# Kernel optimization log

Measured on AMD Instinct MI355X. Metric: run time of the kernel, lower is better.

Reference implementation:

```python
import jax, jax.numpy as jnp
import numpy as np

# Model dims
E, K, D, F = 8, 2, 1024, 2048   # num_experts, top_k, d_model, d_ff
B, S = 2, 1024                  # batch, seq -> T = 2048 tokens


def setup_inputs() -> dict:
    key = jax.random.key(0)
    k1, k2, k3, k4 = jax.random.split(key, 4)
    hidden = jax.random.normal(k1, (B, S, D), dtype=jnp.float32)
    gate_logits = jax.random.normal(k2, (B * S, E), dtype=jnp.float32)
    # Expert FFN params: expert_e(x) = silu(x @ W1[e]) @ W2[e]
    W1 = jax.random.normal(k3, (E, D, F), dtype=jnp.float32) * 0.02
    W2 = jax.random.normal(k4, (E, F, D), dtype=jnp.float32) * 0.02
    return {"hidden": hidden, "gate_logits": gate_logits, "W1": W1, "W2": W2}


def reference(hidden, gate_logits, W1, W2):
    b, s, d = hidden.shape
    x = hidden.reshape(-1, d)                                  # [T, D]
    # Router: softmax -> top-k -> renormalize (gate_logits path of forward)
    probs = jax.nn.softmax(gate_logits, axis=-1)               # [T, E]
    topk_w, topk_idx = jax.lax.top_k(probs, K)                 # [T, K]
    topk_w = topk_w / jnp.sum(topk_w, axis=-1, keepdims=True)
    # Combine weights as a dense [T, E] map (top_k indices are distinct)
    tok_w = jnp.sum(jax.nn.one_hot(topk_idx, E, dtype=topk_w.dtype)
                    * topk_w[..., None], axis=1)               # [T, E]
    # Grouped expert FFN, expressed densely over the expert axis; the
    # combine weights zero out non-selected experts, so the math equals the
    # original gather -> per-expert GEMM -> weighted scatter-combine.
    h = jax.nn.silu(jnp.einsum('td,edf->tef', x, W1))          # [T, E, F]
    y = jnp.einsum('tef,efd->ted', h, W2)                      # [T, E, D]
    out = jnp.einsum('te,ted->td', tok_w, y)                   # [T, D]
    return out.reshape(b, s, d)
```

## Files before the change

kernel.cpp:

```cpp
#include <hip/hip_runtime.h>
#include <hip/hip_bf16.h>

#define E_N 8
#define D_DIM 1024
#define F_DIM 2048
#define T_N 2048
#define BM 128
#define BN 128
#define BK 32
#define LDP 40

typedef unsigned short u16;
typedef unsigned int u32;
typedef float floatx4 __attribute__((ext_vector_type(4)));
typedef short bf16x8v __attribute__((ext_vector_type(8)));

__device__ __forceinline__ u16 f2bf(float f) {
    union { float f; u32 u; } v; v.f = f;
    u32 r = v.u + 0x7FFFu + ((v.u >> 16) & 1u);
    return (u16)(r >> 16);
}

__global__ void router_kernel(const float* __restrict__ gl,
                              int* __restrict__ cnt, int* __restrict__ base,
                              int* __restrict__ slot_tok, int* __restrict__ tok_slot,
                              float* __restrict__ tok_w) {
    __shared__ int scnt[E_N];
    __shared__ int sbase[E_N];
    const int tid = threadIdx.x;
    if (tid < E_N) scnt[tid] = 0;
    __syncthreads();
    int e0a[8], e1a[8], p0a[8], p1a[8];
    float w0a[8];
#pragma unroll
    for (int i = 0; i < 8; ++i) {
        const int t = tid + i * 256;
        const float4* gp = (const float4*)(gl + (size_t)t * E_N);
        const float4 x0 = gp[0], x1 = gp[1];
        float l[E_N] = {x0.x, x0.y, x0.z, x0.w, x1.x, x1.y, x1.z, x1.w};
        int e0 = 0; float m0 = l[0];
#pragma unroll
        for (int e = 1; e < E_N; ++e) if (l[e] > m0) { m0 = l[e]; e0 = e; }
        int e1 = -1; float m1 = -1e30f;
#pragma unroll
        for (int e = 0; e < E_N; ++e) if (e != e0 && l[e] > m1) { m1 = l[e]; e1 = e; }
        const float p = __expf(m1 - m0);
        w0a[i] = 1.0f / (1.0f + p);
        e0a[i] = e0; e1a[i] = e1;
        p0a[i] = atomicAdd(&scnt[e0], 1);
        p1a[i] = atomicAdd(&scnt[e1], 1);
    }
    __syncthreads();
    if (tid == 0) {
        int s = 0;
        for (int e = 0; e < E_N; ++e) { sbase[e] = s; base[e] = s; cnt[e] = scnt[e]; s += scnt[e]; }
    }
    __syncthreads();
#pragma unroll
    for (int i = 0; i < 8; ++i) {
        const int t = tid + i * 256;
        const int s0 = sbase[e0a[i]] + p0a[i];
        const int s1 = sbase[e1a[i]] + p1a[i];
        slot_tok[s0] = t; slot_tok[s1] = t;
        tok_slot[2 * t] = s0; tok_slot[2 * t + 1] = s1;
        tok_w[2 * t] = w0a[i]; tok_w[2 * t + 1] = 1.0f - w0a[i];
    }
}

__global__ __launch_bounds__(256)
void gemm1_kernel(const float* __restrict__ X, const float* __restrict__ W1,
                  const int* __restrict__ cnt, const int* __restrict__ base,
                  const int* __restrict__ slot_tok, u16* __restrict__ h) {
    const int e = blockIdx.z, mt = blockIdx.y, ft = blockIdx.x;
    const int cnt_e = cnt[e];
    if (mt * BM >= cnt_e) return;
    const int base_e = base[e];
    __shared__ __align__(16) u16 Alds[BM][LDP];
    __shared__ __align__(16) u16 Blds[BN][LDP];
    const int tid = threadIdx.x;
    const int ar = tid >> 1, ah = tid & 1;
    const int arow_g = mt * BM + ar;
    const int tok = (arow_g < cnt_e) ? slot_tok[base_e + arow_g] : 0;
    const float* aptr = X + (size_t)tok * D_DIM + ah * 16;
    const int bfc = tid & 127, bh = tid >> 7;
    const float* bptr = W1 + (size_t)e * D_DIM * F_DIM + (size_t)(bh * 16) * F_DIM
                        + (size_t)ft * BN + bfc;
    const int wid = tid >> 6, lane = tid & 63;
    const int wm = (wid >> 1) * 64, wn = (wid & 1) * 64;
    const int lr = lane & 15, lk = (lane >> 4) * 8;
    floatx4 acc[4][4];
    const floatx4 zero = {0.f, 0.f, 0.f, 0.f};
#pragma unroll
    for (int i = 0; i < 4; ++i)
#pragma unroll
        for (int j = 0; j < 4; ++j) acc[i][j] = zero;

    for (int kt = 0; kt < D_DIM / BK; ++kt) {
        const int k0 = kt * BK;
        float4 av[4];
#pragma unroll
        for (int c = 0; c < 4; ++c) av[c] = *(const float4*)(aptr + k0 + c * 4);
        float bv[16];
#pragma unroll
        for (int kk = 0; kk < 16; ++kk) bv[kk] = bptr[(size_t)(k0 + kk) * F_DIM];
        __syncthreads();
        u32 ua[8], ub[8];
#pragma unroll
        for (int c = 0; c < 4; ++c) {
            ua[2 * c]     = (u32)f2bf(av[c].x) | ((u32)f2bf(av[c].y) << 16);
            ua[2 * c + 1] = (u32)f2bf(av[c].z) | ((u32)f2bf(av[c].w) << 16);
        }
#pragma unroll
        for (int j = 0; j < 8; ++j)
            ub[j] = (u32)f2bf(bv[2 * j]) | ((u32)f2bf(bv[2 * j + 1]) << 16);
        u32* adst = (u32*)&Alds[ar][ah * 16];
        *(uint4*)(adst)     = make_uint4(ua[0], ua[1], ua[2], ua[3]);
        *(uint4*)(adst + 4) = make_uint4(ua[4], ua[5], ua[6], ua[7]);
        u32* bdst = (u32*)&Blds[bfc][bh * 16];
        *(uint4*)(bdst)     = make_uint4(ub[0], ub[1], ub[2], ub[3]);
        *(uint4*)(bdst + 4) = make_uint4(ub[4], ub[5], ub[6], ub[7]);
        __syncthreads();
        bf16x8v afr[4], bfr[4];
#pragma unroll
        for (int mi = 0; mi < 4; ++mi) afr[mi] = *(const bf16x8v*)&Alds[wm + mi * 16 + lr][lk];
#pragma unroll
        for (int ni = 0; ni < 4; ++ni) bfr[ni] = *(const bf16x8v*)&Blds[wn + ni * 16 + lr][lk];
#pragma unroll
        for (int mi = 0; mi < 4; ++mi)
#pragma unroll
            for (int ni = 0; ni < 4; ++ni)
                acc[mi][ni] = __builtin_amdgcn_mfma_f32_16x16x32_bf16(afr[mi], bfr[ni], acc[mi][ni], 0, 0, 0);
    }
#pragma unroll
    for (int mi = 0; mi < 4; ++mi) {
#pragma unroll
        for (int r = 0; r < 4; ++r) {
            const int row_t = wm + mi * 16 + ((lane >> 4) << 2) + r;
            const int row_g = mt * BM + row_t;
            if (row_g < cnt_e) {
                u16* hp = h + (size_t)(base_e + row_g) * F_DIM + (size_t)ft * BN + wn + lr;
#pragma unroll
                for (int ni = 0; ni < 4; ++ni) {
                    const float v = acc[mi][ni][r];
                    const float s = v / (1.0f + __expf(-v));
                    hp[ni * 16] = f2bf(s);
                }
            }
        }
    }
}

__global__ __launch_bounds__(256)
void gemm2_kernel(const u16* __restrict__ h, const float* __restrict__ W2,
                  const int* __restrict__ cnt, const int* __restrict__ base,
                  float* __restrict__ y) {
    const int e = blockIdx.z, mt = blockIdx.y, dt = blockIdx.x;
    const int cnt_e = cnt[e];
    if (mt * BM >= cnt_e) return;
    const int base_e = base[e];
    __shared__ __align__(16) u16 Alds[BM][LDP];
    __shared__ __align__(16) u16 Blds[BN][LDP];
    const int tid = threadIdx.x;
    const int ar = tid >> 1, ah = tid & 1;
    int arow = mt * BM + ar; if (arow >= cnt_e) arow = cnt_e - 1;
    const u16* aptr = h + (size_t)(base_e + arow) * F_DIM + ah * 16;
    const int bfc = tid & 127, bh = tid >> 7;
    const float* bptr = W2 + (size_t)e * F_DIM * D_DIM + (size_t)(bh * 16) * D_DIM
                        + (size_t)dt * BN + bfc;
    const int wid = tid >> 6, lane = tid & 63;
    const int wm = (wid >> 1) * 64, wn = (wid & 1) * 64;
    const int lr = lane & 15, lk = (lane >> 4) * 8;
    floatx4 acc[4][4];
    const floatx4 zero = {0.f, 0.f, 0.f, 0.f};
#pragma unroll
    for (int i = 0; i < 4; ++i)
#pragma unroll
        for (int j = 0; j < 4; ++j) acc[i][j] = zero;

    for (int kt = 0; kt < F_DIM / BK; ++kt) {
        const int k0 = kt * BK;
        const uint4 a0 = *(const uint4*)(aptr + k0);
        const uint4 a1 = *(const uint4*)(aptr + k0 + 8);
        float bv[16];
#pragma unroll
        for (int kk = 0; kk < 16; ++kk) bv[kk] = bptr[(size_t)(k0 + kk) * D_DIM];
        __syncthreads();
        u32 ub[8];
#pragma unroll
        for (int j = 0; j < 8; ++j)
            ub[j] = (u32)f2bf(bv[2 * j]) | ((u32)f2bf(bv[2 * j + 1]) << 16);
        u32* adst = (u32*)&Alds[ar][ah * 16];
        *(uint4*)(adst)     = a0;
        *(uint4*)(adst + 4) = a1;
        u32* bdst = (u32*)&Blds[bfc][bh * 16];
        *(uint4*)(bdst)     = make_uint4(ub[0], ub[1], ub[2], ub[3]);
        *(uint4*)(bdst + 4) = make_uint4(ub[4], ub[5], ub[6], ub[7]);
        __syncthreads();
        bf16x8v afr[4], bfr[4];
#pragma unroll
        for (int mi = 0; mi < 4; ++mi) afr[mi] = *(const bf16x8v*)&Alds[wm + mi * 16 + lr][lk];
#pragma unroll
        for (int ni = 0; ni < 4; ++ni) bfr[ni] = *(const bf16x8v*)&Blds[wn + ni * 16 + lr][lk];
#pragma unroll
        for (int mi = 0; mi < 4; ++mi)
#pragma unroll
            for (int ni = 0; ni < 4; ++ni)
                acc[mi][ni] = __builtin_amdgcn_mfma_f32_16x16x32_bf16(afr[mi], bfr[ni], acc[mi][ni], 0, 0, 0);
    }
#pragma unroll
    for (int mi = 0; mi < 4; ++mi) {
#pragma unroll
        for (int r = 0; r < 4; ++r) {
            const int row_t = wm + mi * 16 + ((lane >> 4) << 2) + r;
            const int row_g = mt * BM + row_t;
            if (row_g < cnt_e) {
                float* yp = y + (size_t)(base_e + row_g) * D_DIM + (size_t)dt * BN + wn + lr;
#pragma unroll
                for (int ni = 0; ni < 4; ++ni) yp[ni * 16] = acc[mi][ni][r];
            }
        }
    }
}

__global__ void combine_kernel(const float* __restrict__ y, const int* __restrict__ tok_slot,
                               const float* __restrict__ tok_w, float* __restrict__ out) {
    const int t = blockIdx.x, tid = threadIdx.x;
    const int s0 = tok_slot[2 * t], s1 = tok_slot[2 * t + 1];
    const float w0 = tok_w[2 * t], w1 = tok_w[2 * t + 1];
    const float4 a = *(const float4*)(y + (size_t)s0 * D_DIM + tid * 4);
    const float4 b = *(const float4*)(y + (size_t)s1 * D_DIM + tid * 4);
    float4 o;
    o.x = w0 * a.x + w1 * b.x;
    o.y = w0 * a.y + w1 * b.y;
    o.z = w0 * a.z + w1 * b.z;
    o.w = w0 * a.w + w1 * b.w;
    *(float4*)(out + (size_t)t * D_DIM + tid * 4) = o;
}

extern "C" void kernel_launch(void* const* d_in, const int* in_sizes, int n_in,
                              void* d_out, int out_size, void* d_ws, size_t ws_size,
                              hipStream_t stream) {
    const float* hidden = (const float*)d_in[0];
    const float* gl     = (const float*)d_in[1];
    const float* W1     = (const float*)d_in[2];
    const float* W2     = (const float*)d_in[3];
    float* out = (float*)d_out;

    char* ws = (char*)d_ws;
    int* cnt      = (int*)ws;
    int* basep    = cnt + 8;
    int* slot_tok = basep + 8;
    int* tok_slot = slot_tok + 4096;
    float* tok_w  = (float*)(tok_slot + 4096);
    u16* h   = (u16*)(ws + (1 << 16));
    float* y = (float*)(ws + (1 << 16) + (size_t)4096 * F_DIM * 2);

    router_kernel<<<1, 256, 0, stream>>>(gl, cnt, basep, slot_tok, tok_slot, tok_w);
    gemm1_kernel<<<dim3(F_DIM / BN, T_N / BM, E_N), 256, 0, stream>>>(hidden, W1, cnt, basep, slot_tok, h);
    gemm2_kernel<<<dim3(D_DIM / BN, T_N / BM, E_N), 256, 0, stream>>>(h, W2, cnt, basep, y);
    combine_kernel<<<T_N, 256, 0, stream>>>(y, tok_slot, tok_w, out);
}
```

Baseline: 311.8 us.

## Pre-convert weights to transposed bf16 and stage GEMM tiles via direct-to-LDS loads

Adds a gather kernel that writes routed tokens to bf16, plus kernels that convert and transpose W1/W2 to bf16 K-major layout. The two GEMMs are merged into one templated kernel that uses global_load_lds with an XOR-swizzled LDS layout and a BK=64 tile. GEMM2 is split over K into two halves, and the combine kernel sums the halves. The aim is to remove per-tile fp32 conversion and strided weight loads from the GEMM loops. The cost is extra conversion passes over the full weights on every call and more workspace traffic.

```diff
diff --git a/kernel.cpp b/kernel.cpp
--- a/kernel.cpp
+++ b/kernel.cpp
@@ -5,10 +5,7 @@
 #define D_DIM 1024
 #define F_DIM 2048
 #define T_N 2048
-#define BM 128
-#define BN 128
-#define BK 32
-#define LDP 40
+#define NSLOT 4096
 
 typedef unsigned short u16;
 typedef unsigned int u32;
@@ -19,6 +16,11 @@
     union { float f; u32 u; } v; v.f = f;
     u32 r = v.u + 0x7FFFu + ((v.u >> 16) & 1u);
     return (u16)(r >> 16);
+}
+
+__device__ __forceinline__ void gll16(const void* g, void* l) {
+    __builtin_amdgcn_global_load_lds((const __attribute__((address_space(1))) void*)g,
+                                     (__attribute__((address_space(3))) void*)l, 16, 0, 0);
 }
 
 __global__ void router_kernel(const float* __restrict__ gl,
@@ -67,27 +69,69 @@
     }
 }
 
-__global__ __launch_bounds__(256)
-void gemm1_kernel(const float* __restrict__ X, const float* __restrict__ W1,
-                  const int* __restrict__ cnt, const int* __restrict__ base,
-                  const int* __restrict__ slot_tok, u16* __restrict__ h) {
-    const int e = blockIdx.z, mt = blockIdx.y, ft = blockIdx.x;
+__global__ __launch_bounds__(256) void gather_x_kernel(const float* __restrict__ X,
+                                                       const int* __restrict__ slot_tok,
+                                                       u16* __restrict__ Xg) {
+    const int s = blockIdx.x, t = threadIdx.x;
+    const int tok = slot_tok[s];
+    const float4 v = *(const float4*)(X + (size_t)tok * D_DIM + t * 4);
+    union { u16 o[4]; uint2 q; } u;
+    u.o[0] = f2bf(v.x); u.o[1] = f2bf(v.y); u.o[2] = f2bf(v.z); u.o[3] = f2bf(v.w);
+    *(uint2*)(Xg + (size_t)s * D_DIM + t * 4) = u.q;
+}
+
+__global__ __launch_bounds__(256) void cvt_t_kernel(const float* __restrict__ src,
+                                                    u16* __restrict__ dst, int R, int C) {
+    const int e = blockIdx.z;
+    const int r0 = blockIdx.y << 6, c0 = blockIdx.x << 6;
+    const int t = threadIdx.x;
+    const int n = t & 63, kq = t >> 6;
+    const float* s = src + (size_t)e * R * C + (size_t)(r0 + kq * 16) * C + (c0 + n);
+    union { u16 v[16]; uint4 q[2]; } u;
+#pragma unroll
+    for (int i = 0; i < 16; ++i) u.v[i] = f2bf(s[(size_t)i * C]);
+    u16* d = dst + (size_t)e * R * C + (size_t)(c0 + n) * R + (r0 + kq * 16);
+    *(uint4*)d = u.q[0];
+    *(uint4*)(d + 8) = u.q[1];
+}
+
+template<bool G1>
+__global__ __launch_bounds__(256) void moe_gemm_kernel(
+        const u16* __restrict__ A, const u16* __restrict__ B,
+        const int* __restrict__ cnt, const int* __restrict__ basep,
+        u16* __restrict__ hout, float* __restrict__ yout) {
+    constexpr int KA = G1 ? D_DIM : F_DIM;
+    constexpr int KB = KA;
+    constexpr int KIT = 16;
+    const int e  = G1 ? blockIdx.z : (blockIdx.z >> 1);
+    const int kh = G1 ? 0 : (blockIdx.z & 1);
+    const int mt = blockIdx.y;
+    const int nt = blockIdx.x;
     const int cnt_e = cnt[e];
-    if (mt * BM >= cnt_e) return;
-    const int base_e = base[e];
-    __shared__ __align__(16) u16 Alds[BM][LDP];
-    __shared__ __align__(16) u16 Blds[BN][LDP];
+    if (mt * 128 >= cnt_e) return;
+    const int m0 = basep[e] + mt * 128;
+    const int vm = cnt_e - mt * 128;
+
+    __shared__ __align__(16) u16 Alds[8192];
+    __shared__ __align__(16) u16 Blds[8192];
+
     const int tid = threadIdx.x;
-    const int ar = tid >> 1, ah = tid & 1;
-    const int arow_g = mt * BM + ar;
-    const int tok = (arow_g < cnt_e) ? slot_tok[base_e + arow_g] : 0;
-    const float* aptr = X + (size_t)tok * D_DIM + ah * 16;
-    const int bfc = tid & 127, bh = tid >> 7;
-    const float* bptr = W1 + (size_t)e * D_DIM * F_DIM + (size_t)(bh * 16) * F_DIM
-                        + (size_t)ft * BN + bfc;
     const int wid = tid >> 6, lane = tid & 63;
+    const int l3 = lane >> 3, l7 = lane & 7;
+    const int stgRow = wid * 8 + l3;
+    const int stgCol = ((l7 ^ l3) << 3);
+
+    const u16* aS = A + (size_t)(m0 + stgRow) * KA + kh * (F_DIM / 2) + stgCol;
+    const u16* bS = B + (size_t)e * ((size_t)D_DIM * F_DIM)
+                      + (size_t)(nt * 128 + stgRow) * KB + kh * (F_DIM / 2) + stgCol;
+
     const int wm = (wid >> 1) * 64, wn = (wid & 1) * 64;
-    const int lr = lane & 15, lk = (lane >> 4) * 8;
+    const int lr = lane & 15, lq = lane >> 4;
+    const int aoff = (wm + lr) * 64;
+    const int boff = (wn + lr) * 64;
+    const int sw0 = ((lq)     ^ l7) << 3;
+    const int sw1 = ((lq + 4) ^ l7) << 3;
+
     floatx4 acc[4][4];
     const floatx4 zero = {0.f, 0.f, 0.f, 0.f};
 #pragma unroll
@@ -95,145 +139,80 @@
 #pragma unroll
         for (int j = 0; j < 4; ++j) acc[i][j] = zero;
 
-    for (int kt = 0; kt < D_DIM / BK; ++kt) {
-        const int k0 = kt * BK;
-        float4 av[4];
-#pragma unroll
-        for (int c = 0; c < 4; ++c) av[c] = *(const float4*)(aptr + k0 + c * 4);
-        float bv[16];
-#pragma unroll
-        for (int kk = 0; kk < 16; ++kk) bv[kk] = bptr[(size_t)(k0 + kk) * F_DIM];
+    for (int kt = 0; kt < KIT; ++kt) {
+#pragma unroll
+        for (int c = 0; c < 4; ++c) {
+            gll16(aS + (size_t)(c * 32) * KA, &Alds[c * 2048 + wid * 512]);
+            gll16(bS + (size_t)(c * 32) * KB, &Blds[c * 2048 + wid * 512]);
+        }
+        aS += 64; bS += 64;
         __syncthreads();
-        u32 ua[8], ub[8];
-#pragma unroll
-        for (int c = 0; c < 4; ++c) {
-            ua[2 * c]     = (u32)f2bf(av[c].x) | ((u32)f2bf(av[c].y) << 16);
-            ua[2 * c + 1] = (u32)f2bf(av[c].z) | ((u32)f2bf(av[c].w) << 16);
+#pragma unroll
+        for (int ks = 0; ks < 2; ++ks) {
+            const int sw = ks ? sw1 : sw0;
+            bf16x8v af[4], bfv[4];
+#pragma unroll
+            for (int mi = 0; mi < 4; ++mi) af[mi]  = *(const bf16x8v*)&Alds[aoff + mi * 1024 + sw];
+#pragma unroll
+            for (int ni = 0; ni < 4; ++ni) bfv[ni] = *(const bf16x8v*)&Blds[boff + ni * 1024 + sw];
+#pragma unroll
+            for (int mi = 0; mi < 4; ++mi)
+#pragma unroll
+                for (int ni = 0; ni < 4; ++ni)
+                    acc[mi][ni] = __builtin_amdgcn_mfma_f32_16x16x32_bf16(af[mi], bfv[ni], acc[mi][ni], 0, 0, 0);
         }
-#pragma unroll
-        for (int j = 0; j < 8; ++j)
-            ub[j] = (u32)f2bf(bv[2 * j]) | ((u32)f2bf(bv[2 * j + 1]) << 16);
-        u32* adst = (u32*)&Alds[ar][ah * 16];
-        *(uint4*)(adst)     = make_uint4(ua[0], ua[1], ua[2], ua[3]);
-        *(uint4*)(adst + 4) = make_uint4(ua[4], ua[5], ua[6], ua[7]);
-        u32* bdst = (u32*)&Blds[bfc][bh * 16];
-        *(uint4*)(bdst)     = make_uint4(ub[0], ub[1], ub[2], ub[3]);
-        *(uint4*)(bdst + 4) = make_uint4(ub[4], ub[5], ub[6], ub[7]);
         __syncthreads();
-        bf16x8v afr[4], bfr[4];
-#pragma unroll
-        for (int mi = 0; mi < 4; ++mi) afr[mi] = *(const bf16x8v*)&Alds[wm + mi * 16 + lr][lk];
-#pragma unroll
-        for (int ni = 0; ni < 4; ++ni) bfr[ni] = *(const bf16x8v*)&Blds[wn + ni * 16 + lr][lk];
+    }
+
+    if constexpr (G1) {
 #pragma unroll
         for (int mi = 0; mi < 4; ++mi)
 #pragma unroll
-            for (int ni = 0; ni < 4; ++ni)
-                acc[mi][ni] = __builtin_amdgcn_mfma_f32_16x16x32_bf16(afr[mi], bfr[ni], acc[mi][ni], 0, 0, 0);
-    }
-#pragma unroll
-    for (int mi = 0; mi < 4; ++mi) {
-#pragma unroll
-        for (int r = 0; r < 4; ++r) {
-            const int row_t = wm + mi * 16 + ((lane >> 4) << 2) + r;
-            const int row_g = mt * BM + row_t;
-            if (row_g < cnt_e) {
-                u16* hp = h + (size_t)(base_e + row_g) * F_DIM + (size_t)ft * BN + wn + lr;
-#pragma unroll
-                for (int ni = 0; ni < 4; ++ni) {
-                    const float v = acc[mi][ni][r];
-                    const float s = v / (1.0f + __expf(-v));
-                    hp[ni * 16] = f2bf(s);
+            for (int r = 0; r < 4; ++r) {
+                const int rl = wm + mi * 16 + lq * 4 + r;
+                if (rl < vm) {
+                    u16* hp = hout + (size_t)(m0 + rl) * F_DIM + nt * 128 + wn + lr;
+#pragma unroll
+                    for (int ni = 0; ni < 4; ++ni) {
+                        const float v = acc[mi][ni][r];
+                        hp[ni * 16] = f2bf(v / (1.0f + __expf(-v)));
+                    }
                 }
             }
-        }
-    }
-}
-
-__global__ __launch_bounds__(256)
-void gemm2_kernel(const u16* __restrict__ h, const float* __restrict__ W2,
-                  const int* __restrict__ cnt, const int* __restrict__ base,
-                  float* __restrict__ y) {
-    const int e = blockIdx.z, mt = blockIdx.y, dt = blockIdx.x;
-    const int cnt_e = cnt[e];
-    if (mt * BM >= cnt_e) return;
-    const int base_e = base[e];
-    __shared__ __align__(16) u16 Alds[BM][LDP];
-    __shared__ __align__(16) u16 Blds[BN][LDP];
-    const int tid = threadIdx.x;
-    const int ar = tid >> 1, ah = tid & 1;
-    int arow = mt * BM + ar; if (arow >= cnt_e) arow = cnt_e - 1;
-    const u16* aptr = h + (size_t)(base_e + arow) * F_DIM + ah * 16;
-    const int bfc = tid & 127, bh = tid >> 7;
-    const float* bptr = W2 + (size_t)e * F_DIM * D_DIM + (size_t)(bh * 16) * D_DIM
-                        + (size_t)dt * BN + bfc;
-    const int wid = tid >> 6, lane = tid & 63;
-    const int wm = (wid >> 1) * 64, wn = (wid & 1) * 64;
-    const int lr = lane & 15, lk = (lane >> 4) * 8;
-    floatx4 acc[4][4];
-    const floatx4 zero = {0.f, 0.f, 0.f, 0.f};
-#pragma unroll
-    for (int i = 0; i < 4; ++i)
-#pragma unroll
-        for (int j = 0; j < 4; ++j) acc[i][j] = zero;
-
-    for (int kt = 0; kt < F_DIM / BK; ++kt) {
-        const int k0 = kt * BK;
-        const uint4 a0 = *(const uint4*)(aptr + k0);
-        const uint4 a1 = *(const uint4*)(aptr + k0 + 8);
-        float bv[16];
-#pragma unroll
-        for (int kk = 0; kk < 16; ++kk) bv[kk] = bptr[(size_t)(k0 + kk) * D_DIM];
-        __syncthreads();
-        u32 ub[8];
-#pragma unroll
-        for (int j = 0; j < 8; ++j)
-            ub[j] = (u32)f2bf(bv[2 * j]) | ((u32)f2bf(bv[2 * j + 1]) << 16);
-        u32* adst = (u32*)&Alds[ar][ah * 16];
-        *(uint4*)(adst)     = a0;
-        *(uint4*)(adst + 4) = a1;
-        u32* bdst = (u32*)&Blds[bfc][bh * 16];
-        *(uint4*)(bdst)     = make_uint4(ub[0], ub[1], ub[2], ub[3]);
-        *(uint4*)(bdst + 4) = make_uint4(ub[4], ub[5], ub[6], ub[7]);
-        __syncthreads();
-        bf16x8v afr[4], bfr[4];
-#pragma unroll
-        for (int mi = 0; mi < 4; ++mi) afr[mi] = *(const bf16x8v*)&Alds[wm + mi * 16 + lr][lk];
-#pragma unroll
-        for (int ni = 0; ni < 4; ++ni) bfr[ni] = *(const bf16x8v*)&Blds[wn + ni * 16 + lr][lk];
+    } else {
+        float* Y = yout + (size_t)kh * NSLOT * D_DIM;
 #pragma unroll
         for (int mi = 0; mi < 4; ++mi)
 #pragma unroll
-            for (int ni = 0; ni < 4; ++ni)
-                acc[mi][ni] = __builtin_amdgcn_mfma_f32_16x16x32_bf16(afr[mi], bfr[ni], acc[mi][ni], 0, 0, 0);
-    }
-#pragma unroll
-    for (int mi = 0; mi < 4; ++mi) {
-#pragma unroll
-        for (int r = 0; r < 4; ++r) {
-            const int row_t = wm + mi * 16 + ((lane >> 4) << 2) + r;
-            const int row_g = mt * BM + row_t;
-            if (row_g < cnt_e) {
-                float* yp = y + (size_t)(base_e + row_g) * D_DIM + (size_t)dt * BN + wn + lr;
-#pragma unroll
-                for (int ni = 0; ni < 4; ++ni) yp[ni * 16] = acc[mi][ni][r];
+            for (int r = 0; r < 4; ++r) {
+                const int rl = wm + mi * 16 + lq * 4 + r;
+                if (rl < vm) {
+                    float* yp = Y + (size_t)(m0 + rl) * D_DIM + nt * 128 + wn + lr;
+#pragma unroll
+                    for (int ni = 0; ni < 4; ++ni) yp[ni * 16] = acc[mi][ni][r];
+                }
             }
-        }
-    }
-}
-
-__global__ void combine_kernel(const float* __restrict__ y, const int* __restrict__ tok_slot,
-                               const float* __restrict__ tok_w, float* __restrict__ out) {
+    }
+}
+
+__global__ __launch_bounds__(256) void combine_kernel(const float* __restrict__ Y,
+                                                      const int* __restrict__ tok_slot,
+                                                      const float* __restrict__ tok_w,
+                                                      float* __restrict__ out) {
     const int t = blockIdx.x, tid = threadIdx.x;
     const int s0 = tok_slot[2 * t], s1 = tok_slot[2 * t + 1];
     const float w0 = tok_w[2 * t], w1 = tok_w[2 * t + 1];
-    const float4 a = *(const float4*)(y + (size_t)s0 * D_DIM + tid * 4);
-    const float4 b = *(const float4*)(y + (size_t)s1 * D_DIM + tid * 4);
+    const float* y0 = Y;
+    const float* y1 = Y + (size_t)NSLOT * D_DIM;
+    const float4 a0 = *(const float4*)(y0 + (size_t)s0 * D_DIM + tid * 4);
+    const float4 a1 = *(const float4*)(y1 + (size_t)s0 * D_DIM + tid * 4);
+    const float4 b0 = *(const float4*)(y0 + (size_t)s1 * D_DIM + tid * 4);
+    const float4 b1 = *(const float4*)(y1 + (size_t)s1 * D_DIM + tid * 4);
     float4 o;
-    o.x = w0 * a.x + w1 * b.x;
-    o.y = w0 * a.y + w1 * b.y;
-    o.z = w0 * a.z + w1 * b.z;
-    o.w = w0 * a.w + w1 * b.w;
+    o.x = w0 * (a0.x + a1.x) + w1 * (b0.x + b1.x);
+    o.y = w0 * (a0.y + a1.y) + w1 * (b0.y + b1.y);
+    o.z = w0 * (a0.z + a1.z) + w1 * (b0.z + b1.z);
+    o.w = w0 * (a0.w + a1.w) + w1 * (b0.w + b1.w);
     *(float4*)(out + (size_t)t * D_DIM + tid * 4) = o;
 }
 
@@ -247,16 +226,27 @@
     float* out = (float*)d_out;
 
     char* ws = (char*)d_ws;
-    int* cnt      = (int*)ws;
-    int* basep    = cnt + 8;
-    int* slot_tok = basep + 8;
-    int* tok_slot = slot_tok + 4096;
-    float* tok_w  = (float*)(tok_slot + 4096);
-    u16* h   = (u16*)(ws + (1 << 16));
-    float* y = (float*)(ws + (1 << 16) + (size_t)4096 * F_DIM * 2);
+    int* m = (int*)ws;
+    int* cnt      = m;
+    int* basep    = m + 16;
+    int* slot_tok = m + 32;
+    int* tok_slot = m + 32 + 4096;
+    float* tok_w  = (float*)(m + 32 + 8192);
+
+    const size_t YBYTES = (size_t)2 * NSLOT * D_DIM * 4;
+    const size_t HBYTES = (size_t)(NSLOT + 128) * F_DIM * 2;
+    float* Y = (float*)(ws + (1 << 16));
+    u16* h   = (u16*)(ws + (1 << 16) + YBYTES);
+    char* regionR = ws + (1 << 16) + YBYTES + HBYTES;
+    u16* W1T = (u16*)regionR;
+    u16* Xg  = (u16*)(regionR + (size_t)E_N * D_DIM * F_DIM * 2);
+    u16* W2T = (u16*)regionR;
 
     router_kernel<<<1, 256, 0, stream>>>(gl, cnt, basep, slot_tok, tok_slot, tok_w);
-    gemm1_kernel<<<dim3(F_DIM / BN, T_N / BM, E_N), 256, 0, stream>>>(hidden, W1, cnt, basep, slot_tok, h);
-    gemm2_kernel<<<dim3(D_DIM / BN, T_N / BM, E_N), 256, 0, stream>>>(h, W2, cnt, basep, y);
-    combine_kernel<<<T_N, 256, 0, stream>>>(y, tok_slot, tok_w, out);
-}
+    gather_x_kernel<<<NSLOT, 256, 0, stream>>>(hidden, slot_tok, Xg);
+    cvt_t_kernel<<<dim3(F_DIM / 64, D_DIM / 64, E_N), 256, 0, stream>>>(W1, W1T, D_DIM, F_DIM);
+    moe_gemm_kernel<true><<<dim3(F_DIM / 128, 16, E_N), 256, 0, stream>>>(Xg, W1T, cnt, basep, h, nullptr);
+    cvt_t_kernel<<<dim3(D_DIM / 64, F_DIM / 64, E_N), 256, 0, stream>>>(W2, W2T, F_DIM, D_DIM);
+    moe_gemm_kernel<false><<<dim3(D_DIM / 128, 16, E_N * 2), 256, 0, stream>>>(h, W2T, cnt, basep, nullptr, Y);
+    combine_kernel<<<T_N, 256, 0, stream>>>(Y, tok_slot, tok_w, out);
+}
```

New measurement: 275.2 us. 11.7% less time.
